# Kernel tuning notes

Measured on AMD Instinct MI355X. Metric: run time of the kernel, lower is better.

Reference implementation:

```python
import jax, jax.numpy as jnp
import numpy as np

B, T, N = 8, 168, 1024
FD, FS, FF = 16, 32, 8
DL, DG, HE, E = 128, 128, 4, 16384
BN = B * N


def _lstm_last(x, Wih, Whh, bih, bhh):
    # x: (BN, T, FD); PyTorch gate order i, f, g, o
    h0 = jnp.zeros((x.shape[0], Whh.shape[1]), x.dtype)
    def step(carry, xt):
        h, c = carry
        g = xt @ Wih.T + h @ Whh.T + bih + bhh
        i, f, gg, o = jnp.split(g, 4, axis=-1)
        c = jax.nn.sigmoid(f) * c + jax.nn.sigmoid(i) * jnp.tanh(gg)
        h = jax.nn.sigmoid(o) * jnp.tanh(c)
        return (h, c), None
    (h, _), _ = jax.lax.scan(step, (h0, h0), jnp.swapaxes(x, 0, 1))
    return h


def _ln(x, g, b):
    mu = x.mean(-1, keepdims=True)
    v = ((x - mu) ** 2).mean(-1, keepdims=True)
    return (x - mu) / jnp.sqrt(v + 1e-5) * g + b


def _gat(x, src, dst, ea, W, a_src, a_dst, a_edge, We, bias):
    # PyG GATConv: concat=False (mean over heads), edge_dim=1, LeakyReLU(0.2)
    xl = (x @ W.T).reshape(BN, HE, -1)                 # (BN, H, C)
    as_ = jnp.sum(xl * a_src, -1)                      # (BN, H)
    ad_ = jnp.sum(xl * a_dst, -1)
    ep = (ea @ We.T).reshape(-1, HE, xl.shape[-1])     # (Eb, H, C)
    ae_ = jnp.sum(ep * a_edge, -1)                     # (Eb, H)
    alpha = jax.nn.leaky_relu(as_[src] + ad_[dst] + ae_, 0.2)
    amax = jax.ops.segment_max(alpha, dst, num_segments=BN)
    ex = jnp.exp(alpha - amax[dst])
    den = jax.ops.segment_sum(ex, dst, num_segments=BN)
    w = ex / den[dst]                                  # softmax over incoming edges
    out = jax.ops.segment_sum(w[:, :, None] * xl[src], dst, num_segments=BN)
    return out.mean(axis=1) + bias


def _forward(fl, edge_index):
    (dyn, fcst, sta, ew,
     lWih, lWhh, lbih, lbhh, sW, sb, fW, fb, uW, ub,
     g0W, g0as, g0ad, g0ae, g0We, g0b,
     g1W, g1as, g1ad, g1ae, g1We, g1b,
     n0g, n0b, n1g, n1b, oW, ob) = fl
    x = jnp.transpose(dyn, (0, 2, 1, 3)).reshape(BN, T, FD)
    z = _lstm_last(x, lWih, lWhh, lbih, lbhh)
    s = jax.nn.relu(sta.reshape(BN, -1) @ sW.T + sb)
    f = jax.nn.relu(fcst.reshape(BN, -1) @ fW.T + fb)
    h = jax.nn.relu(jnp.concatenate([z, s, f], -1) @ uW.T + ub)
    # batch the graph: B disjoint copies with node offsets
    off = (jnp.arange(B) * N)[:, None]
    src = (edge_index[0][None] + off).reshape(-1)
    dst = (edge_index[1][None] + off).reshape(-1)
    ea = jnp.tile(ew.reshape(-1, 1), (B, 1))           # (B*E, 1)
    # PyG GATConv default add_self_loops=True, fill_value='mean' of incoming edge attrs
    deg = jax.ops.segment_sum(jnp.ones_like(ea), dst, num_segments=BN)
    loop_ea = jax.ops.segment_sum(ea, dst, num_segments=BN) / jnp.maximum(deg, 1.0)
    loops = jnp.arange(BN)
    src = jnp.concatenate([src, loops])
    dst = jnp.concatenate([dst, loops])
    ea = jnp.concatenate([ea, loop_ea], 0)
    # hop 0: relu on delta (not last hop), residual (res_proj=None since DL==DG), LayerNorm
    d0 = jax.nn.relu(_gat(h, src, dst, ea, g0W, g0as, g0ad, g0ae, g0We, g0b))
    h = _ln(h + d0, n0g, n0b)
    # hop 1: last hop, no relu on delta
    d1 = _gat(h, src, dst, ea, g1W, g1as, g1ad, g1ae, g1We, g1b)
    h = _ln(h + d1, n1g, n1b)
    return (h @ oW.T + ob).reshape(B, N)


def setup_inputs():
    key = jax.random.key(0)
    ks = iter(jax.random.split(key, 48))
    def rn(shape, s=0.08):
        return jax.random.normal(next(ks), shape, jnp.float32) * s
    HO = HE * DG  # heads * out_channels
    return dict(
        dynamic_features=rn((B, T, N, FD), 1.0),
        forecast_features=rn((B, N, FF), 1.0),
        static_features=rn((B, N, FS), 1.0),
        edge_index=jax.random.randint(next(ks), (2, E), 0, N),
        edge_weight=jax.random.uniform(next(ks), (E,), jnp.float32),
        lstm_Wih=rn((4 * DL, FD)), lstm_Whh=rn((4 * DL, DL)),
        lstm_bih=rn((4 * DL,)), lstm_bhh=rn((4 * DL,)),
        static_W=rn((DL, FS)), static_b=rn((DL,)),
        fcst_W=rn((DL, FF)), fcst_b=rn((DL,)),
        fusion_W=rn((DL, 3 * DL)), fusion_b=rn((DL,)),
        gat0_W=rn((HO, DL)), gat0_att_src=rn((1, HE, DG)), gat0_att_dst=rn((1, HE, DG)),
        gat0_att_edge=rn((1, HE, DG)), gat0_We=rn((HO, 1)), gat0_bias=rn((DG,)),
        gat1_W=rn((HO, DG)), gat1_att_src=rn((1, HE, DG)), gat1_att_dst=rn((1, HE, DG)),
        gat1_att_edge=rn((1, HE, DG)), gat1_We=rn((HO, 1)), gat1_bias=rn((DG,)),
        ln0_g=jnp.ones((DG,), jnp.float32), ln0_b=jnp.zeros((DG,), jnp.float32),
        ln1_g=jnp.ones((DG,), jnp.float32), ln1_b=jnp.zeros((DG,), jnp.float32),
        out_W=rn((1, DG)), out_b=rn((1,)),
    )


def reference(dynamic_features, forecast_features, static_features, edge_weight,
              lstm_Wih, lstm_Whh, lstm_bih, lstm_bhh, static_W, static_b,
              fcst_W, fcst_b, fusion_W, fusion_b,
              gat0_W, gat0_att_src, gat0_att_dst, gat0_att_edge, gat0_We, gat0_bias,
              gat1_W, gat1_att_src, gat1_att_dst, gat1_att_edge, gat1_We, gat1_bias,
              ln0_g, ln0_b, ln1_g, ln1_b, out_W, out_b, edge_index):
    fl = (dynamic_features, forecast_features, static_features, edge_weight,
          lstm_Wih, lstm_Whh, lstm_bih, lstm_bhh, static_W, static_b,
          fcst_W, fcst_b, fusion_W, fusion_b,
          gat0_W, gat0_att_src, gat0_att_dst, gat0_att_edge, gat0_We, gat0_bias,
          gat1_W, gat1_att_src, gat1_att_dst, gat1_att_edge, gat1_We, gat1_bias,
          ln0_g, ln0_b, ln1_g, ln1_b, out_W, out_b)
    return _forward(fl, edge_index)
```

## Files before the change

### kernel.cpp

```cpp
#include <hip/hip_runtime.h>
#include <hip/hip_bf16.h>
#include <stdint.h>

#define BB 8
#define TT 168
#define NN 1024
#define BN_ 8192
#define FD_ 16
#define EE 16384

typedef short short8 __attribute__((ext_vector_type(8)));
typedef __bf16 bf16x8 __attribute__((ext_vector_type(8)));
typedef float f32x4 __attribute__((ext_vector_type(4)));

#if __has_builtin(__builtin_amdgcn_exp2f)
#define EXP2(x) __builtin_amdgcn_exp2f(x)
#else
#define EXP2(x) exp2f(x)
#endif
#if __has_builtin(__builtin_amdgcn_rcpf)
#define RCPF(x) __builtin_amdgcn_rcpf(x)
#else
#define RCPF(x) (1.f / (x))
#endif
#define L2E 1.4426950408889634f
#define T2E 2.8853900817779268f

static __device__ __forceinline__ float b2f(ushort s) {
    unsigned u = ((unsigned)s) << 16;
    return __builtin_bit_cast(float, u);
}
static __device__ __forceinline__ ushort f2b(float f) {
    unsigned u = __builtin_bit_cast(unsigned, f);
    unsigned lsb = (u >> 16) & 1u;
    u += 0x7fffu + lsb;
    return (ushort)(u >> 16);
}
static __device__ __forceinline__ float sigf(float x) {
    return 1.f / (1.f + __expf(-x));
}
static __device__ __forceinline__ f32x4 mfma16(short8 a, short8 b, f32x4 c) {
    return __builtin_amdgcn_mfma_f32_16x16x32_bf16(
        __builtin_bit_cast(bf16x8, a), __builtin_bit_cast(bf16x8, b), c, 0, 0, 0);
}

#define O_WIH 0
#define O_WHH 8192
#define O_STA 73728
#define O_FCS 335872
#define O_SW  401408
#define O_FW  405504
#define O_UW  406528
#define O_G0W 455680
#define O_G1W 521216
#define O_END 586752

__global__ void cast_kernel(const float* __restrict__ Wih, const float* __restrict__ Whh,
                            const float* __restrict__ sta, const float* __restrict__ fcst,
                            const float* __restrict__ sW, const float* __restrict__ fW,
                            const float* __restrict__ uW, const float* __restrict__ g0W,
                            const float* __restrict__ g1W, ushort* __restrict__ dst) {
    const int i = blockIdx.x * 256 + threadIdx.x;
    if (i >= O_END) return;
    float v;
    if      (i < O_WHH) v = Wih[i - O_WIH];
    else if (i < O_STA) v = Whh[i - O_WHH];
    else if (i < O_FCS) v = sta[i - O_STA];
    else if (i < O_SW)  v = fcst[i - O_FCS];
    else if (i < O_FW)  v = sW[i - O_SW];
    else if (i < O_UW)  v = fW[i - O_FW];
    else if (i < O_G0W) v = uW[i - O_UW];
    else if (i < O_G1W) v = g0W[i - O_G0W];
    else                v = g1W[i - O_G1W];
    dst[i] = f2b(v);
}

__global__ __launch_bounds__(256, 2) void lstm_kernel(
    const float* __restrict__ dyn,
    const ushort* __restrict__ Wih,
    const ushort* __restrict__ Whh,
    const float* __restrict__ bih,
    const float* __restrict__ bhh,
    ushort* __restrict__ zsf)
{
    constexpr int HS = 168;
    __shared__ ushort haug[16 * HS];

    const int tid = threadIdx.x;
    const int blk = blockIdx.x;
    const int b = blk >> 6;
    const int n0 = (blk & 63) << 4;
    const int w = tid >> 6, lane = tid & 63, quad = lane >> 4, m = lane & 15;

    short8 Bf[5][4][2];
    float ci[2], cf[2], cg[2], co[2];
#pragma unroll
    for (int jj = 0; jj < 2; jj++) {
        const int u = (2 * w + jj) * 16 + m;
#pragma unroll
        for (int g = 0; g < 4; g++) {
            const int grow = g * 128 + u;
#pragma unroll
            for (int kt = 0; kt < 4; kt++)
                Bf[kt][g][jj] = *(const short8*)(Whh + grow * 128 + kt * 32 + quad * 8);
            if (quad < 2) Bf[4][g][jj] = *(const short8*)(Wih + grow * 16 + quad * 8);
            else          Bf[4][g][jj] = short8{0, 0, 0, 0, 0, 0, 0, 0};
        }
        ci[jj] = -L2E * (bih[u] + bhh[u]);
        cf[jj] = -L2E * (bih[128 + u] + bhh[128 + u]);
        cg[jj] =  T2E * (bih[256 + u] + bhh[256 + u]);
        co[jj] = -L2E * (bih[384 + u] + bhh[384 + u]);
    }

    float c[2][4];
#pragma unroll
    for (int jj = 0; jj < 2; jj++)
#pragma unroll
        for (int r = 0; r < 4; r++) c[jj][r] = 0.f;

    for (int i = tid; i < 16 * HS; i += 256) haug[i] = 0;
    __syncthreads();

    const int xn = tid >> 4, xf = tid & 15;
    const size_t xbase = (size_t)b * TT * NN * FD_ + (size_t)(n0 + xn) * FD_ + xf;
    float xv = dyn[xbase];

    for (int t = 0; t < TT; t++) {
        haug[xn * HS + 128 + xf] = f2b(xv);
        __syncthreads();
        if (t + 1 < TT) xv = dyn[xbase + (size_t)(t + 1) * NN * FD_];

        f32x4 acc[4][2];
#pragma unroll
        for (int g = 0; g < 4; g++)
#pragma unroll
            for (int jj = 0; jj < 2; jj++) acc[g][jj] = f32x4{0.f, 0.f, 0.f, 0.f};
#pragma unroll
        for (int kt = 0; kt < 5; kt++) {
            short8 a = *(const short8*)&haug[m * HS + kt * 32 + quad * 8];
#pragma unroll
            for (int g = 0; g < 4; g++)
#pragma unroll
                for (int jj = 0; jj < 2; jj++)
                    acc[g][jj] = mfma16(a, Bf[kt][g][jj], acc[g][jj]);
        }
        __syncthreads();

#pragma unroll
        for (int jj = 0; jj < 2; jj++) {
            const int u = (2 * w + jj) * 16 + m;
#pragma unroll
            for (int r = 0; r < 4; r++) {
                const int n = quad * 4 + r;
                const float si = RCPF(1.f + EXP2(fmaf(acc[0][jj][r], -L2E, ci[jj])));
                const float sf = RCPF(1.f + EXP2(fmaf(acc[1][jj][r], -L2E, cf[jj])));
                const float tg = 1.f - 2.f * RCPF(1.f + EXP2(fmaf(acc[2][jj][r], T2E, cg[jj])));
                const float so = RCPF(1.f + EXP2(fmaf(acc[3][jj][r], -L2E, co[jj])));
                const float cc = fmaf(sf, c[jj][r], si * tg);
                c[jj][r] = cc;
                const float tc = 1.f - 2.f * RCPF(1.f + EXP2(T2E * cc));
                const float h = so * tc;
                haug[n * HS + u] = f2b(h);
                if (t == TT - 1) zsf[(size_t)(blk * 16 + n) * 384 + u] = f2b(h);
            }
        }
    }
}

__global__ __launch_bounds__(256) void gemm_kernel(
    const ushort* __restrict__ A, int lda,
    const ushort* __restrict__ Bt, int ldb,
    int Kact, int Ktiles, int Ncols,
    const float* __restrict__ bias, int relu,
    ushort* __restrict__ outb, int osb,
    float* __restrict__ outf, int osf)
{
    const int tid = threadIdx.x;
    const int lane = tid & 63, quad = lane >> 4, m = lane & 15;
    const int wave = blockIdx.x * 4 + (tid >> 6);
    const int ctiles = Ncols >> 4;
    const int r0 = (wave / ctiles) * 16;
    const int c0 = (wave % ctiles) * 16;

    f32x4 acc = f32x4{0.f, 0.f, 0.f, 0.f};
    for (int kt = 0; kt < Ktiles; kt++) {
        const int k = kt * 32 + quad * 8;
        short8 a, bf;
        if (k + 8 <= Kact) {
            a  = *(const short8*)(A  + (size_t)(r0 + m) * lda + k);
            bf = *(const short8*)(Bt + (size_t)(c0 + m) * ldb + k);
        } else {
#pragma unroll
            for (int j = 0; j < 8; j++) {
                a[j]  = (k + j < Kact) ? (short)A[(size_t)(r0 + m) * lda + k + j] : (short)0;
                bf[j] = (k + j < Kact) ? (short)Bt[(size_t)(c0 + m) * ldb + k + j] : (short)0;
            }
        }
        acc = mfma16(a, bf, acc);
    }
    const int col = c0 + m;
    const float bv = bias ? bias[col] : 0.f;
#pragma unroll
    for (int r = 0; r < 4; r++) {
        const int row = r0 + quad * 4 + r;
        float v = acc[r] + bv;
        if (relu) v = fmaxf(v, 0.f);
        outb[(size_t)row * osb + col] = f2b(v);
        if (outf) outf[(size_t)row * osf + col] = v;
    }
}

__global__ void deg_kernel(const int* __restrict__ ei, const float* __restrict__ ew,
                           int* deg0, float* wsum) {
    const int e = blockIdx.x * 256 + threadIdx.x;
    if (e < EE) {
        const int d = ei[EE + e];
        atomicAdd(&deg0[d], 1);
        atomicAdd(&wsum[d], ew[e]);
    }
}

__global__ void scan_kernel(const int* __restrict__ deg0, const float* __restrict__ wsum,
                            int* offs, float* loopea) {
    __shared__ int sc[1024];
    const int t = threadIdx.x;
    const int d = deg0[t];
    sc[t] = d;
    __syncthreads();
    for (int o = 1; o < 1024; o <<= 1) {
        const int v = (t >= o) ? sc[t - o] : 0;
        __syncthreads();
        sc[t] += v;
        __syncthreads();
    }
    offs[t] = sc[t] - d;
    loopea[t] = wsum[t] / fmaxf((float)d, 1.f);
}

__global__ void fill_kernel(const int* __restrict__ ei, const int* __restrict__ offs,
                            int* cursor, int* eidx) {
    const int e = blockIdx.x * 256 + threadIdx.x;
    if (e < EE) {
        const int d = ei[EE + e];
        const int slot = atomicAdd(&cursor[d], 1);
        eidx[offs[d] + slot] = e;
    }
}

__global__ void sedge_kernel(const float* __restrict__ We0, const float* __restrict__ ae0,
                             const float* __restrict__ We1, const float* __restrict__ ae1,
                             float* se) {
    const int tid = threadIdx.x;
    const int lane = tid & 63, head = (tid >> 6) & 3, hop = tid >> 8;
    const float* W = hop ? We1 : We0;
    const float* A = hop ? ae1 : ae0;
    float s = W[head * 128 + lane] * A[head * 128 + lane] +
              W[head * 128 + 64 + lane] * A[head * 128 + 64 + lane];
#pragma unroll
    for (int o = 32; o; o >>= 1) s += __shfl_xor(s, o);
    if (lane == 0) se[hop * 4 + head] = s;
}

__global__ __launch_bounds__(256) void att_kernel(
    const ushort* __restrict__ xl, const float* __restrict__ asrc,
    const float* __restrict__ adst, float* __restrict__ as_, float* __restrict__ ad_) {
    const int lane = threadIdx.x & 63;
    const int wid = blockIdx.x * 4 + (threadIdx.x >> 6);
    const int base = wid * 4;
    const int p = lane >> 2;
    const int dn = p >> 2, h = p & 3;
    const int sub = lane & 3;
    const ushort* row = xl + (size_t)(base + dn) * 512 + h * 128 + sub * 32;
    const float* sv = asrc + h * 128 + sub * 32;
    const float* dv = adst + h * 128 + sub * 32;
    float sa = 0.f, sd = 0.f;
#pragma unroll
    for (int j = 0; j < 4; j++) {
        short8 x8 = *(const short8*)(row + j * 8);
#pragma unroll
        for (int k = 0; k < 8; k++) {
            const float x = b2f((ushort)x8[k]);
            sa = fmaf(x, sv[j * 8 + k], sa);
            sd = fmaf(x, dv[j * 8 + k], sd);
        }
    }
    sa += __shfl_xor(sa, 1); sa += __shfl_xor(sa, 2);
    sd += __shfl_xor(sd, 1); sd += __shfl_xor(sd, 2);
    if (sub == 0) {
        as_[(base + dn) * 4 + h] = sa;
        ad_[(base + dn) * 4 + h] = sd;
    }
}

__global__ __launch_bounds__(256) void gat_kernel(
    float* __restrict__ hF, ushort* __restrict__ hB, const ushort* __restrict__ xl,
    const float* __restrict__ as_, const float* __restrict__ ad_,
    const int* __restrict__ eidx, const int* __restrict__ offs,
    const int* __restrict__ deg0, const float* __restrict__ loopea,
    const int* __restrict__ ei, const float* __restrict__ ew,
    const float* __restrict__ se4, const float* __restrict__ bias,
    const float* __restrict__ lng, const float* __restrict__ lnb, int relu)
{
    const int lane = threadIdx.x & 63;
    const int v = blockIdx.x * 4 + (threadIdx.x >> 6);
    const int b = v >> 10, n = v & 1023;
    const int dg = deg0[n], off = offs[n];

    float se[4], adv[4];
#pragma unroll
    for (int h = 0; h < 4; h++) { se[h] = se4[h]; adv[h] = ad_[v * 4 + h]; }

    const float lea = loopea[n];
    float den[4], pself[4];
#pragma unroll
    for (int h = 0; h < 4; h++) {
        float a = as_[v * 4 + h] + adv[h] + lea * se[h];
        a = (a < 0.f) ? 0.2f * a : a;
        a = fminf(a, 60.f);
        pself[h] = __expf(a);
        den[h] = pself[h];
    }
    for (int i = 0; i < dg; i++) {
        const int e = eidx[off + i];
        const int src = b * 1024 + ei[e];
        const float eaw = ew[e];
#pragma unroll
        for (int h = 0; h < 4; h++) {
            float a = as_[src * 4 + h] + adv[h] + eaw * se[h];
            a = (a < 0.f) ? 0.2f * a : a;
            a = fminf(a, 60.f);
            den[h] += __expf(a);
        }
    }
    float inv[4];
#pragma unroll
    for (int h = 0; h < 4; h++) inv[h] = 1.f / den[h];

    float o0 = 0.f, o1 = 0.f;
#pragma unroll
    for (int h = 0; h < 4; h++) {
        const float wgt = pself[h] * inv[h];
        o0 += wgt * b2f(xl[(size_t)v * 512 + h * 128 + lane]);
        o1 += wgt * b2f(xl[(size_t)v * 512 + h * 128 + 64 + lane]);
    }
    for (int i = 0; i < dg; i++) {
        const int e = eidx[off + i];
        const int src = b * 1024 + ei[e];
        const float eaw = ew[e];
#pragma unroll
        for (int h = 0; h < 4; h++) {
            float a = as_[src * 4 + h] + adv[h] + eaw * se[h];
            a = (a < 0.f) ? 0.2f * a : a;
            a = fminf(a, 60.f);
            const float wgt = __expf(a) * inv[h];
            o0 += wgt * b2f(xl[(size_t)src * 512 + h * 128 + lane]);
            o1 += wgt * b2f(xl[(size_t)src * 512 + h * 128 + 64 + lane]);
        }
    }

    float d0 = o0 * 0.25f + bias[lane];
    float d1 = o1 * 0.25f + bias[64 + lane];
    if (relu) { d0 = fmaxf(d0, 0.f); d1 = fmaxf(d1, 0.f); }
    const float x0 = hF[(size_t)v * 128 + lane] + d0;
    const float x1 = hF[(size_t)v * 128 + 64 + lane] + d1;

    float s = x0 + x1;
#pragma unroll
    for (int o = 32; o; o >>= 1) s += __shfl_xor(s, o);
    const float mu = s * (1.f / 128.f);
    const float e0 = x0 - mu, e1 = x1 - mu;
    float vs = e0 * e0 + e1 * e1;
#pragma unroll
    for (int o = 32; o; o >>= 1) vs += __shfl_xor(vs, o);
    const float r = rsqrtf(vs * (1.f / 128.f) + 1e-5f);
    const float y0 = e0 * r * lng[lane] + lnb[lane];
    const float y1 = e1 * r * lng[64 + lane] + lnb[64 + lane];
    hF[(size_t)v * 128 + lane] = y0;
    hF[(size_t)v * 128 + 64 + lane] = y1;
    hB[(size_t)v * 128 + lane] = f2b(y0);
    hB[(size_t)v * 128 + 64 + lane] = f2b(y1);
}

__global__ void out_kernel(const float* __restrict__ hF, const float* __restrict__ oW,
                           const float* __restrict__ ob, float* __restrict__ out) {
    const int lane = threadIdx.x & 63;
    const int v = blockIdx.x * 4 + (threadIdx.x >> 6);
    float s = hF[(size_t)v * 128 + lane] * oW[lane] +
              hF[(size_t)v * 128 + 64 + lane] * oW[64 + lane];
#pragma unroll
    for (int o = 32; o; o >>= 1) s += __shfl_xor(s, o);
    if (lane == 0) out[v] = s + ob[0];
}

extern "C" void kernel_launch(void* const* d_in, const int* in_sizes, int n_in,
                              void* d_out, int out_size, void* d_ws, size_t ws_size,
                              hipStream_t stream) {
    const float* dyn  = (const float*)d_in[0];
    const float* fcst = (const float*)d_in[1];
    const float* sta  = (const float*)d_in[2];
    const int*   ei   = (const int*)d_in[3];
    const float* ew   = (const float*)d_in[4];
    const float* lWih = (const float*)d_in[5];
    const float* lWhh = (const float*)d_in[6];
    const float* lbih = (const float*)d_in[7];
    const float* lbhh = (const float*)d_in[8];
    const float* sW = (const float*)d_in[9];
    const float* sb = (const float*)d_in[10];
    const float* fW = (const float*)d_in[11];
    const float* fb = (const float*)d_in[12];
    const float* uW = (const float*)d_in[13];
    const float* ub = (const float*)d_in[14];
    const float* g0W  = (const float*)d_in[15];
    const float* g0as = (const float*)d_in[16];
    const float* g0ad = (const float*)d_in[17];
    const float* g0ae = (const float*)d_in[18];
    const float* g0We = (const float*)d_in[19];
    const float* g0b  = (const float*)d_in[20];
    const float* g1W  = (const float*)d_in[21];
    const float* g1as = (const float*)d_in[22];
    const float* g1ad = (const float*)d_in[23];
    const float* g1ae = (const float*)d_in[24];
    const float* g1We = (const float*)d_in[25];
    const float* g1b  = (const float*)d_in[26];
    const float* ln0g = (const float*)d_in[27];
    const float* ln0b = (const float*)d_in[28];
    const float* ln1g = (const float*)d_in[29];
    const float* ln1b = (const float*)d_in[30];
    const float* oW = (const float*)d_in[31];
    const float* ob = (const float*)d_in[32];

    char* p = (char*)d_ws;
    ushort* castB = (ushort*)p; p += (size_t)O_END * 2 + 512;
    ushort* zsf = (ushort*)p;  p += (size_t)BN_ * 384 * 2;
    float*  hF  = (float*)p;   p += (size_t)BN_ * 128 * 4;
    ushort* hB  = (ushort*)p;  p += (size_t)BN_ * 128 * 2;
    ushort* xl  = (ushort*)p;  p += (size_t)BN_ * 512 * 2;
    float*  asb = (float*)p;   p += (size_t)BN_ * 4 * 4;
    float*  adb = (float*)p;   p += (size_t)BN_ * 4 * 4;
    int*    deg0   = (int*)p;   p += 4096;
    float*  wsum   = (float*)p; p += 4096;
    int*    offs   = (int*)p;   p += 4096;
    int*    cursor = (int*)p;   p += 4096;
    float*  loopea = (float*)p; p += 4096;
    int*    eidx   = (int*)p;   p += (size_t)EE * 4;
    float*  se     = (float*)p; p += 256;

    const ushort* WihB = castB + O_WIH;
    const ushort* WhhB = castB + O_WHH;
    const ushort* staB = castB + O_STA;
    const ushort* fcsB = castB + O_FCS;
    const ushort* sWB  = castB + O_SW;
    const ushort* fWB  = castB + O_FW;
    const ushort* uWB  = castB + O_UW;
    const ushort* g0WB = castB + O_G0W;
    const ushort* g1WB = castB + O_G1W;

    hipMemsetAsync(deg0, 0, 4096, stream);
    hipMemsetAsync(wsum, 0, 4096, stream);
    hipMemsetAsync(cursor, 0, 4096, stream);

    cast_kernel<<<(O_END + 255) / 256, 256, 0, stream>>>(lWih, lWhh, sta, fcst, sW, fW,
                                                         uW, g0W, g1W, castB);
    deg_kernel<<<EE / 256, 256, 0, stream>>>(ei, ew, deg0, wsum);
    scan_kernel<<<1, 1024, 0, stream>>>(deg0, wsum, offs, loopea);
    fill_kernel<<<EE / 256, 256, 0, stream>>>(ei, offs, cursor, eidx);
    sedge_kernel<<<1, 512, 0, stream>>>(g0We, g0ae, g1We, g1ae, se);

    lstm_kernel<<<512, 256, 0, stream>>>(dyn, WihB, WhhB, lbih, lbhh, zsf);

    gemm_kernel<<<1024, 256, 0, stream>>>(staB, 32, sWB, 32, 32, 1, 128, sb, 1,
                                          zsf + 128, 384, nullptr, 0);
    gemm_kernel<<<1024, 256, 0, stream>>>(fcsB, 8, fWB, 8, 8, 1, 128, fb, 1,
                                          zsf + 256, 384, nullptr, 0);
    gemm_kernel<<<1024, 256, 0, stream>>>(zsf, 384, uWB, 384, 384, 12, 128, ub, 1,
                                          hB, 128, hF, 128);

    gemm_kernel<<<4096, 256, 0, stream>>>(hB, 128, g0WB, 128, 128, 4, 512, nullptr, 0,
                                          xl, 512, nullptr, 0);
    att_kernel<<<512, 256, 0, stream>>>(xl, g0as, g0ad, asb, adb);
    gat_kernel<<<2048, 256, 0, stream>>>(hF, hB, xl, asb, adb, eidx, offs, deg0, loopea,
                                         ei, ew, se, g0b, ln0g, ln0b, 1);
    gemm_kernel<<<4096, 256, 0, stream>>>(hB, 128, g1WB, 128, 128, 4, 512, nullptr, 0,
                                          xl, 512, nullptr, 0);
    att_kernel<<<512, 256, 0, stream>>>(xl, g1as, g1ad, asb, adb);
    gat_kernel<<<2048, 256, 0, stream>>>(hF, hB, xl, asb, adb, eidx, offs, deg0, loopea,
                                         ei, ew, se + 4, g1b, ln1g, ln1b, 0);

    out_kernel<<<2048, 256, 0, stream>>>(hF, oW, ob, (float*)d_out);
}
```

Baseline: 632.9 us.

## Fuse graph prep, GEMM+attention, output head; double-buffer LSTM hidden state

Merges the degree, scan, fill and edge-score kernels into one single-block prep kernel, so the memsets go away. The LSTM step now double-buffers its hidden-state tile, which removes one barrier per timestep, and the gate maths is rewritten to share reciprocals with a cheaper bf16 rounding. The GAT projection GEMM is fused with the attention dot products. Edge exponentials are precomputed per edge, so aggregation makes a single pass with an unnormalised numerator. The output head is folded into the last GAT kernel, and the static/forecast GEMMs share one launch. The trade-offs are slightly different rounding, a serial single-block prep, and an extra per-edge buffer that reuses the zsf workspace.

```diff
diff --git a/kernel.cpp b/kernel.cpp
--- a/kernel.cpp
+++ b/kernel.cpp
@@ -36,8 +36,9 @@
     u += 0x7fffu + lsb;
     return (ushort)(u >> 16);
 }
-static __device__ __forceinline__ float sigf(float x) {
-    return 1.f / (1.f + __expf(-x));
+static __device__ __forceinline__ ushort f2b_fast(float f) {
+    unsigned u = __builtin_bit_cast(unsigned, f);
+    return (ushort)((u + 0x8000u) >> 16);
 }
 static __device__ __forceinline__ f32x4 mfma16(short8 a, short8 b, f32x4 c) {
     return __builtin_amdgcn_mfma_f32_16x16x32_bf16(
@@ -75,6 +76,55 @@
     dst[i] = f2b(v);
 }
 
+__global__ __launch_bounds__(1024) void prep_kernel(
+    const int* __restrict__ ei, const float* __restrict__ ew,
+    const float* __restrict__ We0, const float* __restrict__ ae0,
+    const float* __restrict__ We1, const float* __restrict__ ae1,
+    int* __restrict__ deg0, int* __restrict__ offs, float* __restrict__ loopea,
+    int* __restrict__ eidx, float* __restrict__ se) {
+    __shared__ int degL[1024];
+    __shared__ float wsL[1024];
+    __shared__ int sc[1024];
+    __shared__ float seL[8];
+    const int t = threadIdx.x;
+    degL[t] = 0; wsL[t] = 0.f;
+    if (t < 8) seL[t] = 0.f;
+    __syncthreads();
+    for (int e = t; e < EE; e += 1024) {
+        const int d = ei[EE + e];
+        atomicAdd(&degL[d], 1);
+        atomicAdd(&wsL[d], ew[e]);
+    }
+    __syncthreads();
+    const int d = degL[t];
+    sc[t] = d;
+    __syncthreads();
+    for (int o = 1; o < 1024; o <<= 1) {
+        const int v = (t >= o) ? sc[t - o] : 0;
+        __syncthreads();
+        sc[t] += v;
+        __syncthreads();
+    }
+    const int excl = sc[t] - d;
+    offs[t] = excl;
+    deg0[t] = d;
+    loopea[t] = wsL[t] / fmaxf((float)d, 1.f);
+    degL[t] = excl;
+    __syncthreads();
+    for (int e = t; e < EE; e += 1024) {
+        const int dd = ei[EE + e];
+        const int slot = atomicAdd(&degL[dd], 1);
+        eidx[slot] = e;
+    }
+    const int g = t >> 7, k = t & 127;
+    const int head = g & 3;
+    const float* W = (g >> 2) ? We1 : We0;
+    const float* A = (g >> 2) ? ae1 : ae0;
+    atomicAdd(&seL[g], W[head * 128 + k] * A[head * 128 + k]);
+    __syncthreads();
+    if (t < 8) se[t] = seL[t];
+}
+
 __global__ __launch_bounds__(256, 2) void lstm_kernel(
     const float* __restrict__ dyn,
     const ushort* __restrict__ Wih,
@@ -84,7 +134,7 @@
     ushort* __restrict__ zsf)
 {
     constexpr int HS = 168;
-    __shared__ ushort haug[16 * HS];
+    __shared__ ushort hbuf[2][16 * HS];
 
     const int tid = threadIdx.x;
     const int blk = blockIdx.x;
@@ -118,17 +168,20 @@
 #pragma unroll
         for (int r = 0; r < 4; r++) c[jj][r] = 0.f;
 
-    for (int i = tid; i < 16 * HS; i += 256) haug[i] = 0;
+    for (int i = tid; i < 2 * 16 * HS; i += 256) ((ushort*)hbuf)[i] = 0;
     __syncthreads();
 
     const int xn = tid >> 4, xf = tid & 15;
     const size_t xbase = (size_t)b * TT * NN * FD_ + (size_t)(n0 + xn) * FD_ + xf;
-    float xv = dyn[xbase];
+    hbuf[0][xn * HS + 128 + xf] = f2b(dyn[xbase]);
+    float xv = dyn[xbase + (size_t)NN * FD_];
+    __syncthreads();
 
     for (int t = 0; t < TT; t++) {
-        haug[xn * HS + 128 + xf] = f2b(xv);
-        __syncthreads();
-        if (t + 1 < TT) xv = dyn[xbase + (size_t)(t + 1) * NN * FD_];
+        const ushort* rb = hbuf[t & 1];
+        ushort* wb = hbuf[(t + 1) & 1];
+        if (t + 1 < TT) wb[xn * HS + 128 + xf] = f2b(xv);
+        if (t + 2 < TT) xv = dyn[xbase + (size_t)(t + 2) * NN * FD_];
 
         f32x4 acc[4][2];
 #pragma unroll
@@ -137,14 +190,13 @@
             for (int jj = 0; jj < 2; jj++) acc[g][jj] = f32x4{0.f, 0.f, 0.f, 0.f};
 #pragma unroll
         for (int kt = 0; kt < 5; kt++) {
-            short8 a = *(const short8*)&haug[m * HS + kt * 32 + quad * 8];
+            short8 a = *(const short8*)&rb[m * HS + kt * 32 + quad * 8];
 #pragma unroll
             for (int g = 0; g < 4; g++)
 #pragma unroll
                 for (int jj = 0; jj < 2; jj++)
                     acc[g][jj] = mfma16(a, Bf[kt][g][jj], acc[g][jj]);
         }
-        __syncthreads();
 
 #pragma unroll
         for (int jj = 0; jj < 2; jj++) {
@@ -152,210 +204,207 @@
 #pragma unroll
             for (int r = 0; r < 4; r++) {
                 const int n = quad * 4 + r;
-                const float si = RCPF(1.f + EXP2(fmaf(acc[0][jj][r], -L2E, ci[jj])));
-                const float sf = RCPF(1.f + EXP2(fmaf(acc[1][jj][r], -L2E, cf[jj])));
-                const float tg = 1.f - 2.f * RCPF(1.f + EXP2(fmaf(acc[2][jj][r], T2E, cg[jj])));
-                const float so = RCPF(1.f + EXP2(fmaf(acc[3][jj][r], -L2E, co[jj])));
-                const float cc = fmaf(sf, c[jj][r], si * tg);
+                const float Di = 1.f + EXP2(fmaf(acc[0][jj][r], -L2E, ci[jj]));
+                const float Df = 1.f + EXP2(fmaf(acc[1][jj][r], -L2E, cf[jj]));
+                const float Eg = EXP2(fmaf(acc[2][jj][r], T2E, cg[jj]));
+                const float Do = 1.f + EXP2(fmaf(acc[3][jj][r], -L2E, co[jj]));
+                const float R  = RCPF(Di * (1.f + Eg));
+                const float sf = RCPF(Df);
+                const float cc = fmaf(sf, c[jj][r], (Eg - 1.f) * R);
                 c[jj][r] = cc;
-                const float tc = 1.f - 2.f * RCPF(1.f + EXP2(T2E * cc));
-                const float h = so * tc;
-                haug[n * HS + u] = f2b(h);
-                if (t == TT - 1) zsf[(size_t)(blk * 16 + n) * 384 + u] = f2b(h);
+                const float Ec = EXP2(T2E * cc);
+                const float h = (Ec - 1.f) * RCPF(Do * (1.f + Ec));
+                wb[n * HS + u] = f2b_fast(h);
+                if (t == TT - 1) zsf[(size_t)(blk * 16 + n) * 384 + u] = f2b_fast(h);
             }
         }
-    }
-}
-
-__global__ __launch_bounds__(256) void gemm_kernel(
-    const ushort* __restrict__ A, int lda,
-    const ushort* __restrict__ Bt, int ldb,
-    int Kact, int Ktiles, int Ncols,
-    const float* __restrict__ bias, int relu,
-    ushort* __restrict__ outb, int osb,
-    float* __restrict__ outf, int osf)
-{
+        __syncthreads();
+    }
+}
+
+__global__ __launch_bounds__(256) void gemm_sf_kernel(
+    const ushort* __restrict__ staB, const ushort* __restrict__ sWB,
+    const float* __restrict__ sb,
+    const ushort* __restrict__ fcsB, const ushort* __restrict__ fWB,
+    const float* __restrict__ fb, ushort* __restrict__ zsf) {
+    const int tid = threadIdx.x;
+    const int lane = tid & 63, quad = lane >> 4, m = lane & 15;
+    int wave = blockIdx.x * 4 + (tid >> 6);
+    const short8 z8 = short8{0, 0, 0, 0, 0, 0, 0, 0};
+    short8 a, bf;
+    int r0, c0, ocol;
+    const float* bias;
+    if (wave < 4096) {
+        r0 = (wave >> 3) * 16; c0 = (wave & 7) * 16; ocol = 128; bias = sb;
+        a  = *(const short8*)(staB + (size_t)(r0 + m) * 32 + quad * 8);
+        bf = *(const short8*)(sWB + (size_t)(c0 + m) * 32 + quad * 8);
+    } else {
+        wave -= 4096;
+        r0 = (wave >> 3) * 16; c0 = (wave & 7) * 16; ocol = 256; bias = fb;
+        a  = (quad == 0) ? *(const short8*)(fcsB + (size_t)(r0 + m) * 8) : z8;
+        bf = (quad == 0) ? *(const short8*)(fWB + (size_t)(c0 + m) * 8) : z8;
+    }
+    f32x4 acc = mfma16(a, bf, f32x4{0.f, 0.f, 0.f, 0.f});
+    const float bv = bias[c0 + m];
+#pragma unroll
+    for (int r = 0; r < 4; r++) {
+        const int row = r0 + quad * 4 + r;
+        zsf[(size_t)row * 384 + ocol + c0 + m] = f2b(fmaxf(acc[r] + bv, 0.f));
+    }
+}
+
+__global__ __launch_bounds__(256) void gemm_fusion_kernel(
+    const ushort* __restrict__ A, const ushort* __restrict__ Bt,
+    const float* __restrict__ bias, ushort* __restrict__ hB, float* __restrict__ hF) {
     const int tid = threadIdx.x;
     const int lane = tid & 63, quad = lane >> 4, m = lane & 15;
     const int wave = blockIdx.x * 4 + (tid >> 6);
-    const int ctiles = Ncols >> 4;
-    const int r0 = (wave / ctiles) * 16;
-    const int c0 = (wave % ctiles) * 16;
-
+    const int r0 = (wave >> 3) * 16, c0 = (wave & 7) * 16;
     f32x4 acc = f32x4{0.f, 0.f, 0.f, 0.f};
-    for (int kt = 0; kt < Ktiles; kt++) {
+#pragma unroll
+    for (int kt = 0; kt < 12; kt++) {
         const int k = kt * 32 + quad * 8;
-        short8 a, bf;
-        if (k + 8 <= Kact) {
-            a  = *(const short8*)(A  + (size_t)(r0 + m) * lda + k);
-            bf = *(const short8*)(Bt + (size_t)(c0 + m) * ldb + k);
-        } else {
-#pragma unroll
-            for (int j = 0; j < 8; j++) {
-                a[j]  = (k + j < Kact) ? (short)A[(size_t)(r0 + m) * lda + k + j] : (short)0;
-                bf[j] = (k + j < Kact) ? (short)Bt[(size_t)(c0 + m) * ldb + k + j] : (short)0;
-            }
-        }
+        short8 a  = *(const short8*)(A + (size_t)(r0 + m) * 384 + k);
+        short8 bf = *(const short8*)(Bt + (size_t)(c0 + m) * 384 + k);
         acc = mfma16(a, bf, acc);
     }
     const int col = c0 + m;
-    const float bv = bias ? bias[col] : 0.f;
+    const float bv = bias[col];
 #pragma unroll
     for (int r = 0; r < 4; r++) {
         const int row = r0 + quad * 4 + r;
-        float v = acc[r] + bv;
-        if (relu) v = fmaxf(v, 0.f);
-        outb[(size_t)row * osb + col] = f2b(v);
-        if (outf) outf[(size_t)row * osf + col] = v;
-    }
-}
-
-__global__ void deg_kernel(const int* __restrict__ ei, const float* __restrict__ ew,
-                           int* deg0, float* wsum) {
-    const int e = blockIdx.x * 256 + threadIdx.x;
-    if (e < EE) {
-        const int d = ei[EE + e];
-        atomicAdd(&deg0[d], 1);
-        atomicAdd(&wsum[d], ew[e]);
-    }
-}
-
-__global__ void scan_kernel(const int* __restrict__ deg0, const float* __restrict__ wsum,
-                            int* offs, float* loopea) {
-    __shared__ int sc[1024];
-    const int t = threadIdx.x;
-    const int d = deg0[t];
-    sc[t] = d;
-    __syncthreads();
-    for (int o = 1; o < 1024; o <<= 1) {
-        const int v = (t >= o) ? sc[t - o] : 0;
-        __syncthreads();
-        sc[t] += v;
-        __syncthreads();
-    }
-    offs[t] = sc[t] - d;
-    loopea[t] = wsum[t] / fmaxf((float)d, 1.f);
-}
-
-__global__ void fill_kernel(const int* __restrict__ ei, const int* __restrict__ offs,
-                            int* cursor, int* eidx) {
-    const int e = blockIdx.x * 256 + threadIdx.x;
-    if (e < EE) {
-        const int d = ei[EE + e];
-        const int slot = atomicAdd(&cursor[d], 1);
-        eidx[offs[d] + slot] = e;
-    }
-}
-
-__global__ void sedge_kernel(const float* __restrict__ We0, const float* __restrict__ ae0,
-                             const float* __restrict__ We1, const float* __restrict__ ae1,
-                             float* se) {
+        const float v = fmaxf(acc[r] + bv, 0.f);
+        hB[(size_t)row * 128 + col] = f2b(v);
+        hF[(size_t)row * 128 + col] = v;
+    }
+}
+
+__global__ __launch_bounds__(256) void gemmatt_kernel(
+    const ushort* __restrict__ hB, const ushort* __restrict__ W,
+    const float* __restrict__ asrc, const float* __restrict__ adst,
+    ushort* __restrict__ xl, float* __restrict__ as_, float* __restrict__ ad_) {
     const int tid = threadIdx.x;
-    const int lane = tid & 63, head = (tid >> 6) & 3, hop = tid >> 8;
-    const float* W = hop ? We1 : We0;
-    const float* A = hop ? ae1 : ae0;
-    float s = W[head * 128 + lane] * A[head * 128 + lane] +
-              W[head * 128 + 64 + lane] * A[head * 128 + 64 + lane];
-#pragma unroll
-    for (int o = 32; o; o >>= 1) s += __shfl_xor(s, o);
-    if (lane == 0) se[hop * 4 + head] = s;
-}
-
-__global__ __launch_bounds__(256) void att_kernel(
-    const ushort* __restrict__ xl, const float* __restrict__ asrc,
-    const float* __restrict__ adst, float* __restrict__ as_, float* __restrict__ ad_) {
-    const int lane = threadIdx.x & 63;
-    const int wid = blockIdx.x * 4 + (threadIdx.x >> 6);
-    const int base = wid * 4;
-    const int p = lane >> 2;
-    const int dn = p >> 2, h = p & 3;
-    const int sub = lane & 3;
-    const ushort* row = xl + (size_t)(base + dn) * 512 + h * 128 + sub * 32;
-    const float* sv = asrc + h * 128 + sub * 32;
-    const float* dv = adst + h * 128 + sub * 32;
-    float sa = 0.f, sd = 0.f;
-#pragma unroll
-    for (int j = 0; j < 4; j++) {
-        short8 x8 = *(const short8*)(row + j * 8);
-#pragma unroll
-        for (int k = 0; k < 8; k++) {
-            const float x = b2f((ushort)x8[k]);
-            sa = fmaf(x, sv[j * 8 + k], sa);
-            sd = fmaf(x, dv[j * 8 + k], sd);
-        }
-    }
-    sa += __shfl_xor(sa, 1); sa += __shfl_xor(sa, 2);
-    sd += __shfl_xor(sd, 1); sd += __shfl_xor(sd, 2);
-    if (sub == 0) {
-        as_[(base + dn) * 4 + h] = sa;
-        ad_[(base + dn) * 4 + h] = sd;
-    }
+    const int lane = tid & 63, quad = lane >> 4, m = lane & 15;
+    const int w = tid >> 6;
+    const int r0 = blockIdx.x * 16;
+    f32x4 acc[8];
+#pragma unroll
+    for (int ct = 0; ct < 8; ct++) acc[ct] = f32x4{0.f, 0.f, 0.f, 0.f};
+#pragma unroll
+    for (int kt = 0; kt < 4; kt++) {
+        const int k = kt * 32 + quad * 8;
+        short8 a = *(const short8*)(hB + (size_t)(r0 + m) * 128 + k);
+#pragma unroll
+        for (int ct = 0; ct < 8; ct++) {
+            short8 bf = *(const short8*)(W + (size_t)(w * 128 + ct * 16 + m) * 128 + k);
+            acc[ct] = mfma16(a, bf, acc[ct]);
+        }
+    }
+    float sa[4] = {0.f, 0.f, 0.f, 0.f}, sd[4] = {0.f, 0.f, 0.f, 0.f};
+#pragma unroll
+    for (int ct = 0; ct < 8; ct++) {
+        const int col = w * 128 + ct * 16 + m;
+        const float av = asrc[col], dv = adst[col];
+#pragma unroll
+        for (int r = 0; r < 4; r++) {
+            const float v = acc[ct][r];
+            xl[(size_t)(r0 + quad * 4 + r) * 512 + col] = f2b(v);
+            sa[r] = fmaf(v, av, sa[r]);
+            sd[r] = fmaf(v, dv, sd[r]);
+        }
+    }
+#pragma unroll
+    for (int o = 1; o < 16; o <<= 1) {
+#pragma unroll
+        for (int r = 0; r < 4; r++) {
+            sa[r] += __shfl_xor(sa[r], o);
+            sd[r] += __shfl_xor(sd[r], o);
+        }
+    }
+    if (m == 0) {
+#pragma unroll
+        for (int r = 0; r < 4; r++) {
+            const int node = r0 + quad * 4 + r;
+            as_[node * 4 + w] = sa[r];
+            ad_[node * 4 + w] = sd[r];
+        }
+    }
+}
+
+__global__ __launch_bounds__(256) void edge_exp_kernel(
+    const int* __restrict__ ei, const float* __restrict__ ew,
+    const float* __restrict__ as_, const float* __restrict__ ad_,
+    const float* __restrict__ se4, float* __restrict__ pexp) {
+    const int idx = blockIdx.x * 256 + threadIdx.x;
+    const int b = idx >> 14, e = idx & (EE - 1);
+    const int src = b * 1024 + ei[e];
+    const int dst = b * 1024 + ei[EE + e];
+    const float eaw = ew[e];
+    const float4 s4 = *(const float4*)(as_ + src * 4);
+    const float4 d4 = *(const float4*)(ad_ + dst * 4);
+    float4 p;
+    float* pp = (float*)&p;
+    const float* s = (const float*)&s4;
+    const float* d = (const float*)&d4;
+#pragma unroll
+    for (int h = 0; h < 4; h++) {
+        float a = s[h] + d[h] + eaw * se4[h];
+        a = (a < 0.f) ? 0.2f * a : a;
+        pp[h] = EXP2(fminf(a, 60.f) * L2E);
+    }
+    *(float4*)(pexp + (size_t)idx * 4) = p;
 }
 
 __global__ __launch_bounds__(256) void gat_kernel(
     float* __restrict__ hF, ushort* __restrict__ hB, const ushort* __restrict__ xl,
     const float* __restrict__ as_, const float* __restrict__ ad_,
+    const float* __restrict__ pexp,
     const int* __restrict__ eidx, const int* __restrict__ offs,
     const int* __restrict__ deg0, const float* __restrict__ loopea,
-    const int* __restrict__ ei, const float* __restrict__ ew,
+    const int* __restrict__ ei,
     const float* __restrict__ se4, const float* __restrict__ bias,
-    const float* __restrict__ lng, const float* __restrict__ lnb, int relu)
-{
+    const float* __restrict__ lng, const float* __restrict__ lnb, int relu,
+    int writeOut, const float* __restrict__ oW, const float* __restrict__ ob,
+    float* __restrict__ out) {
     const int lane = threadIdx.x & 63;
     const int v = blockIdx.x * 4 + (threadIdx.x >> 6);
     const int b = v >> 10, n = v & 1023;
     const int dg = deg0[n], off = offs[n];
 
-    float se[4], adv[4];
-#pragma unroll
-    for (int h = 0; h < 4; h++) { se[h] = se4[h]; adv[h] = ad_[v * 4 + h]; }
-
     const float lea = loopea[n];
-    float den[4], pself[4];
+    const float4 s4 = *(const float4*)(as_ + v * 4);
+    const float4 d4 = *(const float4*)(ad_ + v * 4);
+    const float* sp = (const float*)&s4;
+    const float* dp = (const float*)&d4;
+    float den[4], num0[4], num1[4];
 #pragma unroll
     for (int h = 0; h < 4; h++) {
-        float a = as_[v * 4 + h] + adv[h] + lea * se[h];
+        float a = sp[h] + dp[h] + lea * se4[h];
         a = (a < 0.f) ? 0.2f * a : a;
-        a = fminf(a, 60.f);
-        pself[h] = __expf(a);
-        den[h] = pself[h];
+        const float p = EXP2(fminf(a, 60.f) * L2E);
+        den[h] = p;
+        num0[h] = p * b2f(xl[(size_t)v * 512 + h * 128 + lane]);
+        num1[h] = p * b2f(xl[(size_t)v * 512 + h * 128 + 64 + lane]);
     }
     for (int i = 0; i < dg; i++) {
         const int e = eidx[off + i];
         const int src = b * 1024 + ei[e];
-        const float eaw = ew[e];
+        const float4 p4 = *(const float4*)(pexp + (size_t)(b * EE + e) * 4);
+        const float* p = (const float*)&p4;
+        const ushort* xr = xl + (size_t)src * 512;
 #pragma unroll
         for (int h = 0; h < 4; h++) {
-            float a = as_[src * 4 + h] + adv[h] + eaw * se[h];
-            a = (a < 0.f) ? 0.2f * a : a;
-            a = fminf(a, 60.f);
-            den[h] += __expf(a);
-        }
-    }
-    float inv[4];
-#pragma unroll
-    for (int h = 0; h < 4; h++) inv[h] = 1.f / den[h];
-
+            den[h] += p[h];
+            num0[h] = fmaf(p[h], b2f(xr[h * 128 + lane]), num0[h]);
+            num1[h] = fmaf(p[h], b2f(xr[h * 128 + 64 + lane]), num1[h]);
+        }
+    }
     float o0 = 0.f, o1 = 0.f;
 #pragma unroll
     for (int h = 0; h < 4; h++) {
-        const float wgt = pself[h] * inv[h];
-        o0 += wgt * b2f(xl[(size_t)v * 512 + h * 128 + lane]);
-        o1 += wgt * b2f(xl[(size_t)v * 512 + h * 128 + 64 + lane]);
-    }
-    for (int i = 0; i < dg; i++) {
-        const int e = eidx[off + i];
-        const int src = b * 1024 + ei[e];
-        const float eaw = ew[e];
-#pragma unroll
-        for (int h = 0; h < 4; h++) {
-            float a = as_[src * 4 + h] + adv[h] + eaw * se[h];
-            a = (a < 0.f) ? 0.2f * a : a;
-            a = fminf(a, 60.f);
-            const float wgt = __expf(a) * inv[h];
-            o0 += wgt * b2f(xl[(size_t)src * 512 + h * 128 + lane]);
-            o1 += wgt * b2f(xl[(size_t)src * 512 + h * 128 + 64 + lane]);
-        }
+        const float inv = RCPF(den[h]);
+        o0 = fmaf(num0[h], inv, o0);
+        o1 = fmaf(num1[h], inv, o1);
     }
 
     float d0 = o0 * 0.25f + bias[lane];
@@ -375,21 +424,17 @@
     const float r = rsqrtf(vs * (1.f / 128.f) + 1e-5f);
     const float y0 = e0 * r * lng[lane] + lnb[lane];
     const float y1 = e1 * r * lng[64 + lane] + lnb[64 + lane];
-    hF[(size_t)v * 128 + lane] = y0;
-    hF[(size_t)v * 128 + 64 + lane] = y1;
-    hB[(size_t)v * 128 + lane] = f2b(y0);
-    hB[(size_t)v * 128 + 64 + lane] = f2b(y1);
-}
-
-__global__ void out_kernel(const float* __restrict__ hF, const float* __restrict__ oW,
-                           const float* __restrict__ ob, float* __restrict__ out) {
-    const int lane = threadIdx.x & 63;
-    const int v = blockIdx.x * 4 + (threadIdx.x >> 6);
-    float s = hF[(size_t)v * 128 + lane] * oW[lane] +
-              hF[(size_t)v * 128 + 64 + lane] * oW[64 + lane];
-#pragma unroll
-    for (int o = 32; o; o >>= 1) s += __shfl_xor(s, o);
-    if (lane == 0) out[v] = s + ob[0];
+    if (writeOut) {
+        float t = y0 * oW[lane] + y1 * oW[64 + lane];
+#pragma unroll
+        for (int o = 32; o; o >>= 1) t += __shfl_xor(t, o);
+        if (lane == 0) out[v] = t + ob[0];
+    } else {
+        hF[(size_t)v * 128 + lane] = y0;
+        hF[(size_t)v * 128 + 64 + lane] = y1;
+        hB[(size_t)v * 128 + lane] = f2b(y0);
+        hB[(size_t)v * 128 + 64 + lane] = f2b(y1);
+    }
 }
 
 extern "C" void kernel_launch(void* const* d_in, const int* in_sizes, int n_in,
@@ -438,12 +483,11 @@
     float*  asb = (float*)p;   p += (size_t)BN_ * 4 * 4;
     float*  adb = (float*)p;   p += (size_t)BN_ * 4 * 4;
     int*    deg0   = (int*)p;   p += 4096;
-    float*  wsum   = (float*)p; p += 4096;
     int*    offs   = (int*)p;   p += 4096;
-    int*    cursor = (int*)p;   p += 4096;
     float*  loopea = (float*)p; p += 4096;
     int*    eidx   = (int*)p;   p += (size_t)EE * 4;
     float*  se     = (float*)p; p += 256;
+    float*  pexp   = (float*)zsf;
 
     const ushort* WihB = castB + O_WIH;
     const ushort* WhhB = castB + O_WHH;
@@ -455,36 +499,23 @@
     const ushort* g0WB = castB + O_G0W;
     const ushort* g1WB = castB + O_G1W;
 
-    hipMemsetAsync(deg0, 0, 4096, stream);
-    hipMemsetAsync(wsum, 0, 4096, stream);
-    hipMemsetAsync(cursor, 0, 4096, stream);
-
     cast_kernel<<<(O_END + 255) / 256, 256, 0, stream>>>(lWih, lWhh, sta, fcst, sW, fW,
                                                          uW, g0W, g1W, castB);
-    deg_kernel<<<EE / 256, 256, 0, stream>>>(ei, ew, deg0, wsum);
-    scan_kernel<<<1, 1024, 0, stream>>>(deg0, wsum, offs, loopea);
-    fill_kernel<<<EE / 256, 256, 0, stream>>>(ei, offs, cursor, eidx);
-    sedge_kernel<<<1, 512, 0, stream>>>(g0We, g0ae, g1We, g1ae, se);
+    prep_kernel<<<1, 1024, 0, stream>>>(ei, ew, g0We, g0ae, g1We, g1ae,
+                                        deg0, offs, loopea, eidx, se);
 
     lstm_kernel<<<512, 256, 0, stream>>>(dyn, WihB, WhhB, lbih, lbhh, zsf);
-
-    gemm_kernel<<<1024, 256, 0, stream>>>(staB, 32, sWB, 32, 32, 1, 128, sb, 1,
-                                          zsf + 128, 384, nullptr, 0);
-    gemm_kernel<<<1024, 256, 0, stream>>>(fcsB, 8, fWB, 8, 8, 1, 128, fb, 1,
-                                          zsf + 256, 384, nullptr, 0);
-    gemm_kernel<<<1024, 256, 0, stream>>>(zsf, 384, uWB, 384, 384, 12, 128, ub, 1,
-                                          hB, 128, hF, 128);
-
-    gemm_kernel<<<4096, 256, 0, stream>>>(hB, 128, g0WB, 128, 128, 4, 512, nullptr, 0,
-                                          xl, 512, nullptr, 0);
-    att_kernel<<<512, 256, 0, stream>>>(xl, g0as, g0ad, asb, adb);
-    gat_kernel<<<2048, 256, 0, stream>>>(hF, hB, xl, asb, adb, eidx, offs, deg0, loopea,
-                                         ei, ew, se, g0b, ln0g, ln0b, 1);
-    gemm_kernel<<<4096, 256, 0, stream>>>(hB, 128, g1WB, 128, 128, 4, 512, nullptr, 0,
-                                          xl, 512, nullptr, 0);
-    att_kernel<<<512, 256, 0, stream>>>(xl, g1as, g1ad, asb, adb);
-    gat_kernel<<<2048, 256, 0, stream>>>(hF, hB, xl, asb, adb, eidx, offs, deg0, loopea,
-                                         ei, ew, se + 4, g1b, ln1g, ln1b, 0);
-
-    out_kernel<<<2048, 256, 0, stream>>>(hF, oW, ob, (float*)d_out);
-}
+    gemm_sf_kernel<<<2048, 256, 0, stream>>>(staB, sWB, sb, fcsB, fWB, fb, zsf);
+    gemm_fusion_kernel<<<1024, 256, 0, stream>>>(zsf, uWB, ub, hB, hF);
+
+    gemmatt_kernel<<<512, 256, 0, stream>>>(hB, g0WB, g0as, g0ad, xl, asb, adb);
+    edge_exp_kernel<<<512, 256, 0, stream>>>(ei, ew, asb, adb, se, pexp);
+    gat_kernel<<<2048, 256, 0, stream>>>(hF, hB, xl, asb, adb, pexp, eidx, offs, deg0,
+                                         loopea, ei, se, g0b, ln0g, ln0b, 1,
+                                         0, oW, ob, (float*)d_out);
+    gemmatt_kernel<<<512, 256, 0, stream>>>(hB, g1WB, g1as, g1ad, xl, asb, adb);
+    edge_exp_kernel<<<512, 256, 0, stream>>>(ei, ew, asb, adb, se + 4, pexp);
+    gat_kernel<<<2048, 256, 0, stream>>>(hF, hB, xl, asb, adb, pexp, eidx, offs, deg0,
+                                         loopea, ei, se + 4, g1b, ln1g, ln1b, 0,
+                                         1, oW, ob, (float*)d_out);
+}
```

Result: faster. 580.2 us (-8.3%).
